# Kernel optimization log

Hardware: AMD Instinct MI355X
Metric: run time of the kernel (lower is better)

Reference implementation:

```python
import jax, jax.numpy as jnp
import numpy as np

N, A_IN, A_OUT, X_IN, X_OUT, NNODE = 4, 8, 16, 64, 64, 1024


def setup_inputs() -> dict:
    key = jax.random.key(0)
    ks = jax.random.split(key, 32)
    s = 0.02
    inp = {
        'A': jax.random.normal(ks[0], (N, A_IN, NNODE, NNODE), jnp.float32),
        'X': jax.random.normal(ks[1], (N, NNODE, X_IN), jnp.float32),
    }
    # Linear weights stored as (in, out); torch Linear computes x @ W.T with W (out,in)
    for i, k in zip(range(1, 6), ks[2:7]):
        inp[f'A_W{i}'] = jax.random.normal(k, (A_IN, A_OUT), jnp.float32) * s
    inp['A_W6'] = jax.random.normal(ks[7], (X_IN, A_OUT), jnp.float32) * s
    inp['A_W7'] = jax.random.normal(ks[8], (X_IN, A_OUT), jnp.float32) * s
    inp['A_bias'] = jnp.zeros((A_OUT,), jnp.float32)
    for pfx, base in (('X1', 9), ('X2', 16)):
        inp[f'{pfx}_W1'] = jax.random.normal(ks[base], (X_IN, X_OUT), jnp.float32) * s
        inp[f'{pfx}_W2'] = jax.random.normal(ks[base + 1], (X_IN, X_OUT), jnp.float32) * s
        for j in range(3, 7):
            inp[f'{pfx}_W{j}'] = jax.random.normal(ks[base + j - 1], (A_IN, X_OUT), jnp.float32) * s
        inp[f'{pfx}_bias'] = jnp.zeros((X_OUT,), jnp.float32)
    inp['out_W'] = jax.random.normal(ks[23], (A_OUT * X_OUT, X_OUT), jnp.float32) * s
    inp['out_b'] = jnp.zeros((X_OUT,), jnp.float32)
    return inp


def reference(A, X, A_W1, A_W2, A_W3, A_W4, A_W5, A_W6, A_W7, A_bias,
              X1_W1, X1_W2, X1_W3, X1_W4, X1_W5, X1_W6, X1_bias,
              X2_W1, X2_W2, X2_W3, X2_W4, X2_W5, X2_W6, X2_bias,
              out_W, out_b):
    n = A.shape[-1]
    # diag_part: N, n, 1, A_in
    dp = jnp.transpose(jnp.diagonal(A, axis1=-2, axis2=-1), (0, 2, 1))[:, :, None, :]
    mdp = jnp.mean(dp, axis=1, keepdims=True)                 # N,1,1,A_in
    moc = jnp.transpose(jnp.mean(A, axis=-1), (0, 2, 1))[:, :, None, :]  # N,n,1,A_in
    mall = jnp.mean(moc, axis=1, keepdims=True)               # N,1,1,A_in
    mX = jnp.mean(X, axis=-2, keepdims=True)                  # N,1,x_in

    At = jnp.transpose(A, (0, 2, 3, 1)) @ A_W1                # N,n,n,A_out
    At = At + mall @ A_W2
    t3 = moc @ A_W3                                           # N,n,1,A_out (linear commutes with symmetrize)
    At = At + t3 + jnp.swapaxes(t3, 1, 2)
    t6 = X @ A_W6                                             # N,n,A_out
    At = At + t6[:, :, None, :] + t6[:, None, :, :]
    At = At + (mX @ A_W7)[:, None, :, :]
    At = At + A_bias
    At = At + mdp @ A_W4
    t5 = dp @ A_W5
    At = At + t5 + jnp.swapaxes(t5, 1, 2)

    def x_branch(W1, W2, W3, W4, W5, W6, b):
        r = X @ W1 + mX @ W2 + moc[:, :, 0, :] @ W3 + mall[:, 0, :, :] @ W6 + b
        return r + dp[:, :, 0, :] @ W4 + mdp[:, 0, :, :] @ W5  # N,n,x_out

    X1t = x_branch(X1_W1, X1_W2, X1_W3, X1_W4, X1_W5, X1_W6, X1_bias)
    X2t = x_branch(X2_W1, X2_W2, X2_W3, X2_W4, X2_W5, X2_W6, X2_bias)

    out = jnp.einsum('nijs,njt->nist', At, X2t) / n           # N,n,A_out,x_out
    out = out.reshape(out.shape[0], out.shape[1], -1) @ out_W + out_b
    out = out + X1t
    return jnp.transpose(At, (0, 3, 1, 2)), out
```

## Files before the change

kernel.cpp:

```cpp
#include <hip/hip_runtime.h>


#define NB 4
#define CI 8
#define SO 16
#define XD 64
#define NN 1024

typedef unsigned short u16;
typedef unsigned int u32;
typedef float f32x4 __attribute__((ext_vector_type(4)));
typedef short bf16x8 __attribute__((ext_vector_type(8)));

#define WS_MOC    0x000000u
#define WS_DP     0x020000u
#define WS_CONSTA 0x043000u
#define WS_CX1    0x044000u
#define WS_CX2    0x045000u
#define WS_K1     0x048000u
#define WS_C2     0x04C000u
#define WS_PAIRA  0x050000u
#define WS_PAIRAT 0x090000u
#define WS_X1T    0x0D0000u
#define WS_X2TT   0x1D0000u
#define WS_WGT    0x250000u
#define WS_H      0x260000u
#define WS_XPART  0x264000u
#define WS_S2     0x268000u

__device__ __forceinline__ float bf2f(u16 u){ return __uint_as_float(((u32)u) << 16); }
__device__ __forceinline__ u16 f2bf(float f){
    u32 x = __float_as_uint(f);
    x += 0x7fffu + ((x >> 16) & 1u);
    return (u16)(x >> 16);
}

__global__ __launch_bounds__(256) void k_rowstats(const float* __restrict__ A,
                                                  const float* __restrict__ X,
                                                  float* __restrict__ moc,
                                                  float* __restrict__ dpv,
                                                  float* __restrict__ Xpart)
{
    if (blockIdx.x < NB*CI*NN/4) {
        int wave = threadIdx.x >> 6, lane = threadIdx.x & 63;
        int row = blockIdx.x * 4 + wave;
        int i = row & (NN - 1);
        const float* rp = A + (size_t)row * NN;
        f32x4 v0 = *(const f32x4*)(rp + lane * 16);
        f32x4 v1 = *(const f32x4*)(rp + lane * 16 + 4);
        f32x4 v2 = *(const f32x4*)(rp + lane * 16 + 8);
        f32x4 v3 = *(const f32x4*)(rp + lane * 16 + 12);
        float s = 0.f;
        #pragma unroll
        for (int e = 0; e < 4; e++) s += v0[e] + v1[e] + v2[e] + v3[e];
        #pragma unroll
        for (int off = 32; off; off >>= 1) s += __shfl_down(s, off);
        if (lane == 0) {
            moc[row] = s * (1.f / NN);
            dpv[row] = rp[i];
        }
    } else {
        int idx = blockIdx.x - NB*CI*NN/4;
        int b = idx >> 4, seg = idx & 15;
        int g = threadIdx.x >> 6, x = threadIdx.x & 63;
        __shared__ float red[4][64];
        float s = 0.f;
        #pragma unroll
        for (int k = 0; k < 16; k++) {
            int i = seg*64 + g*16 + k;
            s += X[((size_t)b*NN + i)*XD + x];
        }
        red[g][x] = s;
        __syncthreads();
        if (threadIdx.x < 64)
            Xpart[idx*64 + threadIdx.x] =
                red[0][threadIdx.x]+red[1][threadIdx.x]+red[2][threadIdx.x]+red[3][threadIdx.x];
    }
}

__global__ __launch_bounds__(256) void k_batchstats(
    const float* __restrict__ Xpart,
    const float* __restrict__ moc, const float* __restrict__ dpv,
    const float* __restrict__ AW2, const float* __restrict__ AW4, const float* __restrict__ AW7,
    const float* __restrict__ Abias,
    const float* __restrict__ X1W2, const float* __restrict__ X1W5, const float* __restrict__ X1W6,
    const float* __restrict__ X1b,
    const float* __restrict__ X2W2, const float* __restrict__ X2W5, const float* __restrict__ X2W6,
    const float* __restrict__ X2b,
    float* __restrict__ constA_o, float* __restrict__ cx1_o, float* __restrict__ cx2_o)
{
    int b = blockIdx.x, tid = threadIdx.x;
    __shared__ float sdp[8][32], smoc[8][32];
    __shared__ float mdp_s[8], mall_s[8], mx_s[64];
    {
        int c = tid >> 5, rr = tid & 31;
        float pd = 0.f, pm = 0.f;
        for (int i = rr; i < NN; i += 32) {
            pd += dpv[(b*CI + c)*NN + i];
            pm += moc[(b*CI + c)*NN + i];
        }
        sdp[c][rr] = pd; smoc[c][rr] = pm;
    }
    if (tid < 64) {
        float px = 0.f;
        #pragma unroll
        for (int s = 0; s < 16; s++) px += Xpart[(b*16 + s)*64 + tid];
        mx_s[tid] = px * (1.f/NN);
    }
    __syncthreads();
    if (tid < 8) {
        float sd = 0.f, sm = 0.f;
        for (int k = 0; k < 32; k++) { sd += sdp[tid][k]; sm += smoc[tid][k]; }
        mdp_s[tid] = sd * (1.f/NN); mall_s[tid] = sm * (1.f/NN);
    }
    __syncthreads();
    if (tid < SO) {
        float v = Abias[tid];
        #pragma unroll
        for (int c = 0; c < 8; c++)
            v += mall_s[c]*AW2[c*SO+tid] + mdp_s[c]*AW4[c*SO+tid];
        for (int x = 0; x < 64; x++) v += mx_s[x]*AW7[x*SO+tid];
        constA_o[b*SO + tid] = v;
    }
    if (tid < 64) {
        float v1 = X1b[tid], v2 = X2b[tid];
        for (int x = 0; x < 64; x++) {
            float m = mx_s[x];
            v1 += m*X1W2[x*64+tid];
            v2 += m*X2W2[x*64+tid];
        }
        #pragma unroll
        for (int c = 0; c < 8; c++) {
            v1 += mall_s[c]*X1W6[c*64+tid] + mdp_s[c]*X1W5[c*64+tid];
            v2 += mall_s[c]*X2W6[c*64+tid] + mdp_s[c]*X2W5[c*64+tid];
        }
        cx1_o[b*64+tid] = v1; cx2_o[b*64+tid] = v2;
    }
}

__global__ __launch_bounds__(256) void k_rows(const float* __restrict__ X,
    const float* __restrict__ moc, const float* __restrict__ dpv,
    const float* __restrict__ AW3, const float* __restrict__ AW5, const float* __restrict__ AW6,
    const float* __restrict__ X1W1, const float* __restrict__ X1W3, const float* __restrict__ X1W4,
    const float* __restrict__ X2W1, const float* __restrict__ X2W3, const float* __restrict__ X2W4,
    const float* __restrict__ cx1, const float* __restrict__ cx2,
    float* __restrict__ X1t, u16* __restrict__ X2tT,
    float* __restrict__ pairA, float* __restrict__ pairAT)
{
    int wave = threadIdx.x >> 6, u = threadIdx.x & 63;
    int r = blockIdx.x * 4 + wave;
    int b = r >> 10, i = r & (NN - 1);
    float xv = X[(size_t)r*XD + u];
    float a1 = cx1[b*XD + u], a2 = cx2[b*XD + u];
    int s = u & 15;
    float pa = 0.f;
    for (int x = 0; x < XD; x++) {
        float xx = __shfl(xv, x);
        a1 += xx * X1W1[x*XD + u];
        a2 += xx * X2W1[x*XD + u];
        pa += xx * AW6[x*SO + s];
    }
    #pragma unroll
    for (int c = 0; c < CI; c++) {
        float mv = moc[(b*CI + c)*NN + i];
        float dv = dpv[(b*CI + c)*NN + i];
        a1 += mv*X1W3[c*XD+u] + dv*X1W4[c*XD+u];
        a2 += mv*X2W3[c*XD+u] + dv*X2W4[c*XD+u];
        pa += mv*AW3[c*SO+s] + dv*AW5[c*SO+s];
    }
    X1t[(size_t)r*XD + u] = a1;
    X2tT[((size_t)b*XD + u)*NN + i] = f2bf(a2);
    if (u < SO) {
        pairA[(size_t)r*SO + u] = pa;
        pairAT[((size_t)b*SO + u)*NN + i] = pa;
    }
}

__global__ __launch_bounds__(256) void k_H(const float* __restrict__ pairAT,
                                           const u16* __restrict__ X2tT,
                                           float* __restrict__ H, float* __restrict__ s2)
{
    __shared__ float red[4][64];
    int tid = threadIdx.x;
    int t = tid & 63, g = tid >> 6;
    if (blockIdx.x < 64) {
        int b = blockIdx.x >> 4, s = blockIdx.x & 15;
        const u16* x2 = X2tT + ((size_t)(b*XD) + t)*NN;
        const float* par = pairAT + ((size_t)(b*SO) + s)*NN;
        float h = 0.f;
        for (int i = g*256; i < (g+1)*256; i += 8) {
            bf16x8 v = __builtin_bit_cast(bf16x8, *(const uint4*)(x2 + i));
            f32x4 p0 = *(const f32x4*)(par + i);
            f32x4 p1 = *(const f32x4*)(par + i + 4);
            #pragma unroll
            for (int e = 0; e < 4; e++)
                h += p0[e]*bf2f((u16)v[e]) + p1[e]*bf2f((u16)v[e+4]);
        }
        red[g][t] = h;
        __syncthreads();
        if (tid < 64)
            H[((size_t)(b*SO) + s)*64 + tid] = red[0][tid]+red[1][tid]+red[2][tid]+red[3][tid];
    } else {
        int b = blockIdx.x - 64;
        const u16* x2 = X2tT + ((size_t)(b*XD) + t)*NN;
        float p = 0.f;
        for (int i = g*256; i < (g+1)*256; i += 8) {
            bf16x8 v = __builtin_bit_cast(bf16x8, *(const uint4*)(x2 + i));
            #pragma unroll
            for (int e = 0; e < 8; e++) p += bf2f((u16)v[e]);
        }
        red[g][t] = p;
        __syncthreads();
        if (tid < 64)
            s2[b*64 + tid] = red[0][tid]+red[1][tid]+red[2][tid]+red[3][tid];
    }
}

__global__ __launch_bounds__(256) void k_small2(const float* __restrict__ Wo, const float* __restrict__ AW1,
    const float* __restrict__ constA, const float* __restrict__ H, const float* __restrict__ s2,
    float* __restrict__ K1, float* __restrict__ C2, u16* __restrict__ WGT)
{
    int tid = threadIdx.x;
    if (blockIdx.x < 4) {
        int b = blockIdx.x;
        __shared__ float ls[4][64];
        int t = tid & 63, g = tid >> 6;
        const float* s2b = s2 + b*64;
        float pc = 0.f;
        #pragma unroll
        for (int si = 0; si < 4; si++) {
            int s = g*4 + si;
            float ca = constA[b*SO + s];
            const float* Hs = H + ((size_t)(b*SO) + s)*64;
            float v = 0.f;
            for (int tt = 0; tt < 64; tt++) {
                float w = Wo[(s*64+tt)*64 + t];
                v  += s2b[tt] * w;
                pc += (Hs[tt] + ca*s2b[tt]) * w;
            }
            K1[((size_t)(b*SO) + s)*XD + t] = v;
        }
        ls[g][t] = pc;
        __syncthreads();
        if (tid < 64) C2[b*XD + tid] = (ls[0][tid]+ls[1][tid]+ls[2][tid]+ls[3][tid]) * (1.f/NN);
    } else {
        int o = (blockIdx.x - 4)*256 + tid;
        int u = o >> 9;
        int k = o & 511;
        int c = k >> 6, t = k & 63;
        float v = 0.f;
        #pragma unroll
        for (int s = 0; s < SO; s++) v += AW1[c*SO+s] * Wo[(s*64+t)*64 + u];
        WGT[(size_t)u*512 + k] = f2bf(v);
    }
}

#define LOAD_STEP(ST, A0, A1, BF) { \
    int j0_ = jh*512 + (ST)*32 + lq*8; \
    _Pragma("unroll") \
    for (int c = 0; c < CI; c++) { \
        const float* ar_ = Ab + (size_t)c*NN*NN + j0_; \
        A0[c] = *(const f32x4*)ar_; \
        A1[c] = *(const f32x4*)(ar_ + 4); \
    } \
    BF = __builtin_bit_cast(bf16x8, *(const uint4*)(Xb + j0_)); \
}

#define COMP_STEP(ST, A0, A1, BF) { \
    int j0_ = jh*512 + (ST)*32 + lq*8; \
    _Pragma("unroll") \
    for (int s = 0; s < 4; s++) { \
        const float* pt_ = pairAT + ((size_t)(b*SO) + s4 + s)*NN + j0_; \
        f32x4 p0 = *(const f32x4*)pt_; \
        f32x4 p1 = *(const f32x4*)(pt_ + 4); \
        f32x4 o0, o1; \
        _Pragma("unroll") \
        for (int e = 0; e < 4; e++) { o0[e] = rc[s] + p0[e]; o1[e] = rc[s] + p1[e]; } \
        _Pragma("unroll") \
        for (int c = 0; c < CI; c++) { \
            float wv = W1s[c][s4 + s]; \
            _Pragma("unroll") \
            for (int e = 0; e < 4; e++) { o0[e] += A0[c][e]*wv; o1[e] += A1[c][e]*wv; } \
        } \
        float* op_ = out0 + (((size_t)(b*SO + s4 + s))*NN + i0 + lr)*NN + j0_; \
        __builtin_nontemporal_store(o0, (f32x4*)op_); \
        __builtin_nontemporal_store(o1, (f32x4*)(op_ + 4)); \
    } \
    _Pragma("unroll") \
    for (int c = 0; c < CI; c++) { \
        bf16x8 af; \
        _Pragma("unroll") \
        for (int e = 0; e < 4; e++) { af[e] = (short)f2bf(A0[c][e]); af[e+4] = (short)f2bf(A1[c][e]); } \
        acc[c] = __builtin_amdgcn_mfma_f32_16x16x32_bf16(af, BF, acc[c], 0, 0, 0); \
    } \
}

__global__ __launch_bounds__(512, 2) void k_fused(
    const float* __restrict__ A, const u16* __restrict__ X2tT,
    const float* __restrict__ AW1,
    const float* __restrict__ pairA, const float* __restrict__ pairAT,
    const float* __restrict__ constA,
    const u16* __restrict__ WGT, const float* __restrict__ K1,
    const float* __restrict__ C2, const float* __restrict__ X1t,
    const float* __restrict__ outb,
    float* __restrict__ out0, float* __restrict__ out1)
{
    __shared__ float W1s[CI][SO];
    __shared__ __align__(16) float Gsh[4][CI][64][4];
    __shared__ __align__(16) u16 Gb[16][520];

    int tid = threadIdx.x;
    int wave = tid >> 6, lane = tid & 63;
    int lr = lane & 15, lq = lane >> 4;
    int nt = wave & 3, jh = wave >> 2;
    int b = blockIdx.x >> 6;
    int i0 = (blockIdx.x & 63) * 16;
    int s4 = nt * 4;

    if (tid < CI*SO) W1s[tid >> 4][tid & 15] = AW1[tid];

    float rc[4];
    {
        f32x4 t = *(const f32x4*)(pairA + ((size_t)(b*NN) + i0 + lr)*SO + s4);
        const float* ca = constA + b*SO + s4;
        #pragma unroll
        for (int s = 0; s < 4; s++) rc[s] = t[s] + ca[s];
    }
    __syncthreads();

    const float* Ab = A + ((size_t)b*CI)*NN*NN + (size_t)(i0 + lr)*NN;
    const u16*  Xb = X2tT + ((size_t)(b*XD) + nt*16 + lr)*NN;

    f32x4 acc[CI];
    #pragma unroll
    for (int c = 0; c < CI; c++) acc[c] = (f32x4){0.f,0.f,0.f,0.f};

    f32x4 aA0[CI], aA1[CI], aB0[CI], aB1[CI];
    bf16x8 bfA, bfB;
    LOAD_STEP(0, aA0, aA1, bfA);
    for (int st2 = 0; st2 < 8; st2++) {
        LOAD_STEP(st2*2 + 1, aB0, aB1, bfB);
        COMP_STEP(st2*2, aA0, aA1, bfA);
        if (st2 < 7) LOAD_STEP(st2*2 + 2, aA0, aA1, bfA);
        COMP_STEP(st2*2 + 1, aB0, aB1, bfB);
    }

    if (jh == 1) {
        #pragma unroll
        for (int c = 0; c < CI; c++)
            *(f32x4*)&Gsh[nt][c][lane][0] = acc[c];
    }
    __syncthreads();
    if (jh == 0) {
        #pragma unroll
        for (int c = 0; c < CI; c++) {
            f32x4 g = *(const f32x4*)&Gsh[nt][c][lane][0];
            #pragma unroll
            for (int reg = 0; reg < 4; reg++)
                Gb[lq*4 + reg][c*64 + nt*16 + lr] = f2bf(acc[c][reg] + g[reg]);
        }
    }
    __syncthreads();

    if (jh == 0) {
        f32x4 acc1 = (f32x4){0.f,0.f,0.f,0.f};
        #pragma unroll
        for (int k0 = 0; k0 < 512; k0 += 32) {
            bf16x8 ga = __builtin_bit_cast(bf16x8, *(const uint4*)&Gb[lr][k0 + lq*8]);
            bf16x8 wb = __builtin_bit_cast(bf16x8,
                *(const uint4*)(WGT + (size_t)(nt*16 + lr)*512 + k0 + lq*8));
            acc1 = __builtin_amdgcn_mfma_f32_16x16x32_bf16(ga, wb, acc1, 0, 0, 0);
        }
        int u = nt*16 + lr;
        float k1c[SO];
        #pragma unroll
        for (int s = 0; s < SO; s++) k1c[s] = K1[((size_t)(b*SO) + s)*XD + u];
        float cb = C2[b*XD + u] + outb[u];
        #pragma unroll
        for (int reg = 0; reg < 4; reg++) {
            int ii = i0 + lq*4 + reg;
            const float* pa = pairA + ((size_t)(b*NN) + ii)*SO;
            float s16 = 0.f;
            #pragma unroll
            for (int s = 0; s < SO; s++) s16 += pa[s] * k1c[s];
            out1[((size_t)(b*NN) + ii)*XD + u] =
                (acc1[reg] + s16) * (1.f/NN) + cb
                + X1t[((size_t)(b*NN) + ii)*XD + u];
        }
    }
}

extern "C" void kernel_launch(void* const* d_in, const int* in_sizes, int n_in,
                              void* d_out, int out_size, void* d_ws, size_t ws_size,
                              hipStream_t stream)
{
    const float* A     = (const float*)d_in[0];
    const float* X     = (const float*)d_in[1];
    const float* AW1   = (const float*)d_in[2];
    const float* AW2   = (const float*)d_in[3];
    const float* AW3   = (const float*)d_in[4];
    const float* AW4   = (const float*)d_in[5];
    const float* AW5   = (const float*)d_in[6];
    const float* AW6   = (const float*)d_in[7];
    const float* AW7   = (const float*)d_in[8];
    const float* Abias = (const float*)d_in[9];
    const float* X1W1  = (const float*)d_in[10];
    const float* X1W2  = (const float*)d_in[11];
    const float* X1W3  = (const float*)d_in[12];
    const float* X1W4  = (const float*)d_in[13];
    const float* X1W5  = (const float*)d_in[14];
    const float* X1W6  = (const float*)d_in[15];
    const float* X1b   = (const float*)d_in[16];
    const float* X2W1  = (const float*)d_in[17];
    const float* X2W2  = (const float*)d_in[18];
    const float* X2W3  = (const float*)d_in[19];
    const float* X2W4  = (const float*)d_in[20];
    const float* X2W5  = (const float*)d_in[21];
    const float* X2W6  = (const float*)d_in[22];
    const float* X2b   = (const float*)d_in[23];
    const float* Wo    = (const float*)d_in[24];
    const float* outb  = (const float*)d_in[25];

    char* ws = (char*)d_ws;
    float* moc    = (float*)(ws + WS_MOC);
    float* dpv    = (float*)(ws + WS_DP);
    float* constA = (float*)(ws + WS_CONSTA);
    float* cx1    = (float*)(ws + WS_CX1);
    float* cx2    = (float*)(ws + WS_CX2);
    float* K1     = (float*)(ws + WS_K1);
    float* C2     = (float*)(ws + WS_C2);
    float* pairA  = (float*)(ws + WS_PAIRA);
    float* pairAT = (float*)(ws + WS_PAIRAT);
    float* X1t    = (float*)(ws + WS_X1T);
    u16*   X2tT   = (u16*)(ws + WS_X2TT);
    u16*   WGT    = (u16*)(ws + WS_WGT);
    float* H      = (float*)(ws + WS_H);
    float* Xpart  = (float*)(ws + WS_XPART);
    float* s2     = (float*)(ws + WS_S2);

    float* out0 = (float*)d_out;
    float* out1 = out0 + (size_t)NB*SO*NN*NN;

    k_rowstats<<<dim3(NB*CI*NN/4 + 64), dim3(256), 0, stream>>>(A, X, moc, dpv, Xpart);
    k_batchstats<<<dim3(NB), dim3(256), 0, stream>>>(Xpart, moc, dpv,
        AW2, AW4, AW7, Abias, X1W2, X1W5, X1W6, X1b, X2W2, X2W5, X2W6, X2b,
        constA, cx1, cx2);
    k_rows<<<dim3(NB*NN/4), dim3(256), 0, stream>>>(X, moc, dpv,
        AW3, AW5, AW6, X1W1, X1W3, X1W4, X2W1, X2W3, X2W4, cx1, cx2,
        X1t, X2tT, pairA, pairAT);
    k_H<<<dim3(68), dim3(256), 0, stream>>>(pairAT, X2tT, H, s2);
    k_small2<<<dim3(132), dim3(256), 0, stream>>>(Wo, AW1, constA, H, s2, K1, C2, WGT);
    k_fused<<<dim3(NB*NN/16), dim3(512), 0, stream>>>(A, X2tT, AW1,
        pairA, pairAT, constA, WGT, K1, C2, X1t, outb, out0, out1);
}
```

Baseline: 562.6 us.

## Split fused kernel j-range across 16 waves and drop manual double buffering

Doubles the block to 1024 threads so each of four wave groups covers a quarter of the j columns, replacing the register double-buffered load/compute pipeline with a simple loop. The partial MFMA accumulators are reduced serially through shared memory over extra barriers. Output stores change from nontemporal to ordinary stores. The aim is to hide memory latency with more resident waves instead of software prefetch, at the cost of more synchronisation, a longer reduction, and tighter register limits from launch_bounds(1024,4).

```diff
diff --git a/kernel.cpp b/kernel.cpp
--- a/kernel.cpp
+++ b/kernel.cpp
@@ -255,47 +255,7 @@
     }
 }
 
-#define LOAD_STEP(ST, A0, A1, BF) { \
-    int j0_ = jh*512 + (ST)*32 + lq*8; \
-    _Pragma("unroll") \
-    for (int c = 0; c < CI; c++) { \
-        const float* ar_ = Ab + (size_t)c*NN*NN + j0_; \
-        A0[c] = *(const f32x4*)ar_; \
-        A1[c] = *(const f32x4*)(ar_ + 4); \
-    } \
-    BF = __builtin_bit_cast(bf16x8, *(const uint4*)(Xb + j0_)); \
-}
-
-#define COMP_STEP(ST, A0, A1, BF) { \
-    int j0_ = jh*512 + (ST)*32 + lq*8; \
-    _Pragma("unroll") \
-    for (int s = 0; s < 4; s++) { \
-        const float* pt_ = pairAT + ((size_t)(b*SO) + s4 + s)*NN + j0_; \
-        f32x4 p0 = *(const f32x4*)pt_; \
-        f32x4 p1 = *(const f32x4*)(pt_ + 4); \
-        f32x4 o0, o1; \
-        _Pragma("unroll") \
-        for (int e = 0; e < 4; e++) { o0[e] = rc[s] + p0[e]; o1[e] = rc[s] + p1[e]; } \
-        _Pragma("unroll") \
-        for (int c = 0; c < CI; c++) { \
-            float wv = W1s[c][s4 + s]; \
-            _Pragma("unroll") \
-            for (int e = 0; e < 4; e++) { o0[e] += A0[c][e]*wv; o1[e] += A1[c][e]*wv; } \
-        } \
-        float* op_ = out0 + (((size_t)(b*SO + s4 + s))*NN + i0 + lr)*NN + j0_; \
-        __builtin_nontemporal_store(o0, (f32x4*)op_); \
-        __builtin_nontemporal_store(o1, (f32x4*)(op_ + 4)); \
-    } \
-    _Pragma("unroll") \
-    for (int c = 0; c < CI; c++) { \
-        bf16x8 af; \
-        _Pragma("unroll") \
-        for (int e = 0; e < 4; e++) { af[e] = (short)f2bf(A0[c][e]); af[e+4] = (short)f2bf(A1[c][e]); } \
-        acc[c] = __builtin_amdgcn_mfma_f32_16x16x32_bf16(af, BF, acc[c], 0, 0, 0); \
-    } \
-}
-
-__global__ __launch_bounds__(512, 2) void k_fused(
+__global__ __launch_bounds__(1024, 4) void k_fused(
     const float* __restrict__ A, const u16* __restrict__ X2tT,
     const float* __restrict__ AW1,
     const float* __restrict__ pairA, const float* __restrict__ pairAT,
@@ -312,7 +272,7 @@
     int tid = threadIdx.x;
     int wave = tid >> 6, lane = tid & 63;
     int lr = lane & 15, lq = lane >> 4;
-    int nt = wave & 3, jh = wave >> 2;
+    int nt = wave & 3, jq = wave >> 2;
     int b = blockIdx.x >> 6;
     int i0 = (blockIdx.x & 63) * 16;
     int s4 = nt * 4;
@@ -335,34 +295,81 @@
     #pragma unroll
     for (int c = 0; c < CI; c++) acc[c] = (f32x4){0.f,0.f,0.f,0.f};
 
-    f32x4 aA0[CI], aA1[CI], aB0[CI], aB1[CI];
-    bf16x8 bfA, bfB;
-    LOAD_STEP(0, aA0, aA1, bfA);
-    for (int st2 = 0; st2 < 8; st2++) {
-        LOAD_STEP(st2*2 + 1, aB0, aB1, bfB);
-        COMP_STEP(st2*2, aA0, aA1, bfA);
-        if (st2 < 7) LOAD_STEP(st2*2 + 2, aA0, aA1, bfA);
-        COMP_STEP(st2*2 + 1, aB0, aB1, bfB);
-    }
-
-    if (jh == 1) {
+    for (int st = 0; st < 8; st++) {
+        int j0 = jq*256 + st*32 + lq*8;
+        f32x4 a0[CI], a1[CI];
+        #pragma unroll
+        for (int c = 0; c < CI; c++) {
+            const float* ar = Ab + (size_t)c*NN*NN + j0;
+            a0[c] = *(const f32x4*)ar;
+            a1[c] = *(const f32x4*)(ar + 4);
+        }
+        bf16x8 bfr = __builtin_bit_cast(bf16x8, *(const uint4*)(Xb + j0));
+        #pragma unroll
+        for (int s = 0; s < 4; s++) {
+            const float* pt = pairAT + ((size_t)(b*SO) + s4 + s)*NN + j0;
+            f32x4 p0 = *(const f32x4*)pt;
+            f32x4 p1 = *(const f32x4*)(pt + 4);
+            f32x4 o0, o1;
+            #pragma unroll
+            for (int e = 0; e < 4; e++) { o0[e] = rc[s] + p0[e]; o1[e] = rc[s] + p1[e]; }
+            #pragma unroll
+            for (int c = 0; c < CI; c++) {
+                float wv = W1s[c][s4 + s];
+                #pragma unroll
+                for (int e = 0; e < 4; e++) { o0[e] += a0[c][e]*wv; o1[e] += a1[c][e]*wv; }
+            }
+            float* op = out0 + (((size_t)(b*SO + s4 + s))*NN + i0 + lr)*NN + j0;
+            *(f32x4*)op = o0;
+            *(f32x4*)(op + 4) = o1;
+        }
+        #pragma unroll
+        for (int c = 0; c < CI; c++) {
+            bf16x8 af;
+            #pragma unroll
+            for (int e = 0; e < 4; e++) { af[e] = (short)f2bf(a0[c][e]); af[e+4] = (short)f2bf(a1[c][e]); }
+            acc[c] = __builtin_amdgcn_mfma_f32_16x16x32_bf16(af, bfr, acc[c], 0, 0, 0);
+        }
+    }
+
+    if (jq == 3) {
         #pragma unroll
         for (int c = 0; c < CI; c++)
             *(f32x4*)&Gsh[nt][c][lane][0] = acc[c];
     }
     __syncthreads();
-    if (jh == 0) {
+    if (jq == 2) {
         #pragma unroll
         for (int c = 0; c < CI; c++) {
             f32x4 g = *(const f32x4*)&Gsh[nt][c][lane][0];
             #pragma unroll
+            for (int e = 0; e < 4; e++) g[e] += acc[c][e];
+            *(f32x4*)&Gsh[nt][c][lane][0] = g;
+        }
+    }
+    __syncthreads();
+    if (jq == 1) {
+        #pragma unroll
+        for (int c = 0; c < CI; c++) {
+            f32x4 g = *(const f32x4*)&Gsh[nt][c][lane][0];
+            #pragma unroll
+            for (int e = 0; e < 4; e++) g[e] += acc[c][e];
+            *(f32x4*)&Gsh[nt][c][lane][0] = g;
+        }
+    }
+    __syncthreads();
+    if (jq == 0) {
+        #pragma unroll
+        for (int c = 0; c < CI; c++) {
+            f32x4 g = *(const f32x4*)&Gsh[nt][c][lane][0];
+            #pragma unroll
             for (int reg = 0; reg < 4; reg++)
                 Gb[lq*4 + reg][c*64 + nt*16 + lr] = f2bf(acc[c][reg] + g[reg]);
         }
     }
     __syncthreads();
 
-    if (jh == 0) {
+    if (jq == 0) {
         f32x4 acc1 = (f32x4){0.f,0.f,0.f,0.f};
         #pragma unroll
         for (int k0 = 0; k0 < 512; k0 += 32) {
@@ -450,6 +457,6 @@
         X1t, X2tT, pairA, pairAT);
     k_H<<<dim3(68), dim3(256), 0, stream>>>(pairAT, X2tT, H, s2);
     k_small2<<<dim3(132), dim3(256), 0, stream>>>(Wo, AW1, constA, H, s2, K1, C2, WGT);
-    k_fused<<<dim3(NB*NN/16), dim3(512), 0, stream>>>(A, X2tT, AW1,
+    k_fused<<<dim3(NB*NN/16), dim3(1024), 0, stream>>>(A, X2tT, AW1,
         pairA, pairAT, constA, WGT, K1, C2, X1t, outb, out0, out1);
 }
```

Result: slower. 803.0 us (+42.7%).
